# Optimization experiments

Measured on AMD Instinct MI355X. Metric: run time of the kernel, lower is better.

The kernel has to match this reference:

```python
import jax, jax.numpy as jnp
import numpy as np

LMAX=4; MMAX=2; L2=25; M2=19; C=64; CE=64; NRBF=600; CUT=5.0
HEADS=8; ACH=32; VCH=16; HMSG=64; HFF=128; G=288; NL=2
AVG_NEI=20.0; AVG_NODES=2000.0
N_NODES=2000; N_EDGES=40000; NSPEC=90
# |m| group of each truncated (edge-frame) coefficient, order l=0..4, m=-min(l,2)..min(l,2)
MG = np.array([0, 1,0,1, 2,1,0,1,2, 2,1,0,1,2, 2,1,0,1,2])
# l of each full SH coefficient (25 total)
LOC = np.array([0] + [1]*3 + [2]*5 + [3]*7 + [4]*9)

def silu(x):
    return x * jax.nn.sigmoid(x)

def rms_norm_sh(x, w):
    # x: [N, 25, C]; w: [5, C] per-degree affine weight (rms_norm_sh)
    ms = jnp.mean(x * x, axis=1, keepdims=True)
    return x * jax.lax.rsqrt(ms + 1e-6) * w[LOC][None]

def setup_inputs() -> dict:
    key = jax.random.key(0)
    ks = iter(jax.random.split(key, 64))
    def rn(shape, scale):
        return jax.random.normal(next(ks), shape, dtype=jnp.float32) * scale
    inp = {}
    inp['edge_vectors'] = rn((N_EDGES, 3), 1.5)
    inp['wigner'] = rn((N_EDGES, M2, L2), 0.2)
    inp['wigner_inv'] = rn((N_EDGES, L2, M2), 0.2)
    inp['species_embed'] = rn((NSPEC, C), 1.0)
    inp['edge_species_embed'] = rn((NSPEC, 2 * CE), 1.0)
    DIN = NRBF + 2 * CE  # 728
    inp['deg_W1'] = rn((DIN, 128), DIN ** -0.5)
    inp['deg_b1'] = jnp.zeros((128,), jnp.float32)
    inp['deg_W2'] = rn((128, M2 * C), 128 ** -0.5)
    inp['deg_b2'] = jnp.zeros((M2 * C,), jnp.float32)
    inp['norm1_w'] = jnp.ones((NL, 5, C), jnp.float32)
    inp['rad_W1'] = rn((NL, DIN, 128), DIN ** -0.5)
    inp['rad_b1'] = jnp.zeros((NL, 128), jnp.float32)
    inp['rad_W2'] = rn((NL, 128, 3 * 2 * C), 128 ** -0.5)
    inp['rad_b2'] = jnp.ones((NL, 3 * 2 * C), jnp.float32)
    inp['so2_W'] = rn((NL, 3, 2 * C, HMSG), (2 * C) ** -0.5)
    inp['alpha_W'] = rn((NL, HMSG, HEADS * ACH), HMSG ** -0.5)
    inp['alpha_vec'] = rn((NL, HEADS, ACH), ACH ** -0.5)
    inp['value_W'] = rn((NL, 3, HMSG, HEADS * VCH), HMSG ** -0.5)
    inp['proj_W'] = rn((NL, 3, HEADS * VCH, C), (HEADS * VCH) ** -0.5)
    inp['norm2_w'] = jnp.ones((NL, 5, C), jnp.float32)
    inp['ffn_W1'] = rn((NL, C, HFF), C ** -0.5)
    inp['ffn_b1'] = jnp.zeros((NL, HFF), jnp.float32)
    inp['ffn_W2'] = rn((NL, HFF, C), HFF ** -0.5)
    inp['to_grid'] = rn((G, L2), L2 ** -0.5)
    inp['from_grid'] = rn((L2, G), G ** -0.5)
    inp['final_norm_w'] = jnp.ones((5, C), jnp.float32)
    inp['en_W1'] = rn((C, HFF), C ** -0.5)
    inp['en_b1'] = jnp.zeros((HFF,), jnp.float32)
    inp['en_W2'] = rn((HFF, 1), HFF ** -0.5)
    inp['en_b2'] = jnp.zeros((1,), jnp.float32)
    inp['node_species'] = jax.random.randint(next(ks), (N_NODES,), 0, NSPEC, dtype=jnp.int32)
    inp['senders'] = jax.random.randint(next(ks), (N_EDGES,), 0, N_NODES, dtype=jnp.int32)
    inp['receivers'] = jax.random.randint(next(ks), (N_EDGES,), 0, N_NODES, dtype=jnp.int32)
    inp['n_node'] = jnp.array([N_NODES], jnp.int32)
    return inp

def reference(edge_vectors, wigner, wigner_inv, species_embed, edge_species_embed,
              deg_W1, deg_b1, deg_W2, deg_b2, norm1_w, rad_W1, rad_b1, rad_W2, rad_b2,
              so2_W, alpha_W, alpha_vec, value_W, proj_W, norm2_w, ffn_W1, ffn_b1, ffn_W2,
              to_grid, from_grid, final_norm_w, en_W1, en_b1, en_W2, en_b2,
              node_species, senders, receivers, n_node):
    N = node_species.shape[0]
    E = senders.shape[0]
    mg = jnp.asarray(MG)
    # Gaussian RBF distance expansion (rbf_width=2.0)
    d = jnp.sqrt(jnp.sum(edge_vectors * edge_vectors, axis=-1) + 1e-12)
    offs = jnp.linspace(0.0, CUT, NRBF)
    std = 2.0 * (CUT / (NRBF - 1))
    rbf = jnp.exp(-0.5 * ((d[:, None] - offs[None, :]) / std) ** 2)  # [E, 600]
    # shared atom-edge embedding concat
    ne = edge_species_embed[node_species]
    se, re = jnp.split(ne, 2, axis=-1)
    ee = jnp.concatenate([rbf, se[senders], re[receivers]], axis=1)  # [E, 728]
    # initial node features: species embedding on l=0 component
    x = jnp.zeros((N, L2, C), dtype=edge_vectors.dtype).at[:, 0, :].set(species_embed[node_species])
    # edge degree embedding: radial MLP -> edge-frame coeffs -> rotate back -> scatter
    h = silu(ee @ deg_W1 + deg_b1) @ deg_W2 + deg_b2
    deg = jnp.einsum('elm,emc->elc', wigner_inv, h.reshape(E, M2, C))  # [E,25,C]
    x = x + jax.ops.segment_sum(deg, receivers, num_segments=N) / AVG_NEI
    for i in range(NL):
        # --- SO2 equivariant graph attention ---
        res = x
        xn = rms_norm_sh(x, norm1_w[i])
        msg = jnp.concatenate([xn[senders], xn[receivers]], axis=-1)      # [E,25,2C]
        msg = jnp.einsum('eml,elc->emc', wigner, msg)                     # rotate to edge frame [E,19,2C]
        rad = (silu(ee @ rad_W1[i] + rad_b1[i]) @ rad_W2[i] + rad_b2[i]).reshape(E, MMAX + 1, 2 * C)
        msg = msg * rad[:, mg]                                            # per-|m| radial modulation
        h = jnp.einsum('emc,mco->emo', msg, so2_W[i][mg])                 # SO2 conv [E,19,HMSG]
        a = (silu(h[:, 0, :]) @ alpha_W[i]).reshape(E, HEADS, ACH)        # invariant (m=0) alpha path
        logits = jnp.sum(silu(a) * alpha_vec[i][None], axis=-1)           # [E,HEADS]
        mx = jax.ops.segment_max(logits, receivers, num_segments=N)[receivers]
        ex = jnp.exp(logits - mx)
        den = jax.ops.segment_sum(ex, receivers, num_segments=N)[receivers]
        attn = ex / (den + 1e-12)
        v = jnp.einsum('emo,mov->emv', h, value_W[i][mg]).reshape(E, M2, HEADS, VCH)
        v = (v * attn[:, None, :, None]).reshape(E, M2, HEADS * VCH)
        oe = jnp.einsum('emv,mvc->emc', v, proj_W[i][mg])                 # [E,19,C]
        oe = jnp.einsum('elm,emc->elc', wigner_inv, oe)                   # rotate back [E,25,C]
        x = res + jax.ops.segment_sum(oe, receivers, num_segments=N)
        # --- S2 grid feed-forward ---
        res = x
        xn = rms_norm_sh(x, norm2_w[i])
        g = jnp.einsum('gl,nlc->ngc', to_grid, xn)                        # [N,288,C]
        g = silu(g @ ffn_W1[i] + ffn_b1[i]) @ ffn_W2[i]
        x = res + jnp.einsum('lg,ngc->nlc', from_grid, g)
    # final norm + energy head
    xn = rms_norm_sh(x, final_norm_w)
    g = jnp.einsum('gl,nlc->ngc', to_grid, xn)
    g = silu(g @ en_W1 + en_b1) @ en_W2 + en_b2
    eo = jnp.einsum('lg,ngo->nlo', from_grid, g)
    return eo[:, 0, 0] / AVG_NODES
```

## Files before the change

kernel.cpp:

```cpp
#include <hip/hip_runtime.h>
#include <hip/hip_bf16.h>
#include <math.h>


#define NRBF 600
#define DIN 728
#define GPTS 288
#define CH 8

typedef __attribute__((ext_vector_type(8))) short bf16x8;
typedef __attribute__((ext_vector_type(4))) float f32x4;

__constant__ int d_mg[19] = {0,1,0,1,2,1,0,1,2,2,1,0,1,2,2,1,0,1,2};
__constant__ int d_loc[25] = {0,1,1,1,2,2,2,2,2,3,3,3,3,3,3,3,4,4,4,4,4,4,4,4,4};
__constant__ int d_mg0[5]={0,2,6,11,16};
__constant__ int d_mg1[8]={1,3,5,7,10,12,15,17};
__constant__ int d_mg2[6]={4,8,9,13,14,18};

__device__ inline float silu_f(float v){ return v/(1.0f+__expf(-v)); }
__device__ inline float bf2f(unsigned short u){ return __uint_as_float(((unsigned)u)<<16); }
__device__ inline unsigned short f2bf(float f){
  unsigned b=__float_as_uint(f);
  return (unsigned short)((b + 0x7FFF + ((b>>16)&1)) >> 16);
}

__device__ inline void atomicMaxF(float* addr, float val){
  int* ia=(int*)addr;
  int old=*ia;
  while (__int_as_float(old) < val){
    int assumed=old;
    old = atomicCAS(ia, assumed, __float_as_int(val));
    if (old == assumed) break;
  }
}

__global__ __launch_bounds__(256) void zero_cnt_kernel(int* cnt, int N){
  int i = blockIdx.x*256+threadIdx.x;
  if (i<N) cnt[i]=0;
}
__global__ __launch_bounds__(256) void csr_count_kernel(const int* __restrict__ rcv, int* cnt, int E){
  int i = blockIdx.x*256+threadIdx.x;
  if (i<E) atomicAdd(&cnt[rcv[i]],1);
}
__global__ __launch_bounds__(256) void csr_scan_kernel(const int* __restrict__ cnt,
    int* rowptr, int* fill, int N){
  __shared__ int s_part[256];
  int tid=threadIdx.x;
  int chunk=(N+255)/256;
  int lvals[12];
  int base=tid*chunk;
  int lsum=0;
  for (int i=0;i<chunk && i<12;i++){
    int v=(base+i<N)?cnt[base+i]:0;
    lvals[i]=lsum; lsum+=v;
  }
  s_part[tid]=lsum;
  __syncthreads();
  if (tid==0){
    int run=0;
    for (int t=0;t<256;t++){ int v=s_part[t]; s_part[t]=run; run+=v; }
  }
  __syncthreads();
  int off=s_part[tid];
  for (int i=0;i<chunk && i<12;i++){
    if (base+i<N){ rowptr[base+i]=off+lvals[i]; fill[base+i]=off+lvals[i]; }
  }
  if (tid==255) rowptr[N]=off+lsum;
}
__global__ __launch_bounds__(256) void csr_fill_kernel(const int* __restrict__ rcv,
    int* fill, int* eix, int E){
  int i = blockIdx.x*256+threadIdx.x;
  if (i<E){ int p=atomicAdd(&fill[rcv[i]],1); eix[p]=i; }
}

__global__ __launch_bounds__(256) void wsvb_kernel(const float* __restrict__ so2W,
    const float* __restrict__ valW, unsigned short* __restrict__ wsvb){
  int i=blockIdx.x/3, g=blockIdx.x%3;
  const float* A = so2W + (size_t)i*24576 + g*8192;
  const float* B = valW + (size_t)i*24576 + g*8192;
  unsigned short* C = wsvb + (size_t)blockIdx.x*16384;
  __shared__ float sB[8192];
  for (int j=threadIdx.x;j<2048;j+=256) ((float4*)sB)[j]=((const float4*)B)[j];
  __syncthreads();
  for (int idx=threadIdx.x; idx<16384; idx+=256){
    int k=idx>>7, j=idx&127;
    float acc=0;
    #pragma unroll 4
    for (int o=0;o<64;o++) acc += A[k*64+o]*sB[o*128+j];
    int pos = ((k>>5)*8 + (j>>4))*512 + (((k>>3)&3)*16 + (j&15))*8 + (k&7);
    C[pos]=f2bf(acc);
  }
}

__global__ __launch_bounds__(256) void projb_kernel(const float* __restrict__ pW,
    unsigned short* __restrict__ projb){
  const float* src = pW + (size_t)blockIdx.x*8192;
  unsigned short* dst = projb + (size_t)blockIdx.x*8192;
  for (int idx=threadIdx.x; idx<8192; idx+=256){
    int k=idx>>6, j=idx&63;
    int pos = ((k>>5)*4 + (j>>4))*512 + (((k>>3)&3)*16 + (j&15))*8 + (k&7);
    dst[pos]=f2bf(src[idx]);
  }
}

__global__ __launch_bounds__(256) void packB2g_kernel(const float* __restrict__ src,
    unsigned short* __restrict__ dh, unsigned short* __restrict__ dl, int K, int Nn){
  int ktiles=(K+31)>>5;
  int nnt=Nn>>4;
  int tot=ktiles*nnt*512;
  for (int idx=blockIdx.x*256+threadIdx.x; idx<tot; idx+=gridDim.x*256){
    int f=idx>>9, r=idx&511, lane=r>>3, j=r&7;
    int kt=f/nnt, nt=f-kt*nnt;
    int k=kt*32+(lane>>4)*8+j, c=nt*16+(lane&15);
    float v=(k<K)? src[k*Nn+c] : 0.0f;
    unsigned short h=f2bf(v);
    dh[idx]=h;
    dl[idx]=f2bf(v-bf2f(h));
  }
}

__global__ __launch_bounds__(256) void pack_tg2_kernel(const float* __restrict__ tg,
    unsigned short* __restrict__ tgp){
  int tid=threadIdx.x;
  for (int idx=tid; idx<9216; idx+=256){
    int t=idx>>9, r=idx&511, lane=r>>3, j=r&7;
    int kl=(lane>>4)*8+j, row=t*16+(lane&15);
    float v=(kl<25)? tg[row*25+kl] : 0.0f;
    unsigned short h=f2bf(v);
    tgp[idx]=h;
    tgp[9216+idx]=f2bf(v-bf2f(h));
  }
}

__global__ __launch_bounds__(256) void pack_fg2_kernel(const float* __restrict__ fg,
    unsigned short* __restrict__ fgp){
  int tid=threadIdx.x;
  for (int idx=tid; idx<18432; idx+=256){
    int f=idx>>9, r=idx&511, lane=r>>3, j=r&7;
    int t=f>>1, mt=f&1;
    int row=mt*16+(lane&15), k=(lane>>4)*8+j;
    float v=(row<25 && k<16)? fg[row*288+t*16+k] : 0.0f;
    unsigned short h=f2bf(v);
    fgp[idx]=h;
    fgp[18432+idx]=f2bf(v-bf2f(h));
  }
}

__global__ __launch_bounds__(256) void mlpf_kernel(const float* __restrict__ ev,
    const float* __restrict__ ese, const int* __restrict__ nsp,
    const unsigned short* __restrict__ dw1h, const unsigned short* __restrict__ dw1l,
    const float* __restrict__ db1,
    const unsigned short* __restrict__ dw2h, const unsigned short* __restrict__ dw2l,
    const float* __restrict__ db2,
    const unsigned short* __restrict__ r1h, const unsigned short* __restrict__ r1l,
    const float* __restrict__ rb1,
    const unsigned short* __restrict__ r2h, const unsigned short* __restrict__ r2l,
    const float* __restrict__ rb2,
    const int* __restrict__ snd, const int* __restrict__ rcv, const int* __restrict__ eix,
    int do_deg,
    unsigned short* __restrict__ degout, float* __restrict__ radout, int E){
  int tid=threadIdx.x, wv=tid>>6, lane=tid&63;
  int lanelo=lane&15, khi=lane>>4;
  int p0=blockIdx.x*16;
  __shared__ unsigned short s_eeh[4096], s_eel[4096];
  __shared__ unsigned short s_h1h[2048], s_h1l[2048];
  __shared__ float s_d[16]; __shared__ int s_ss[16], s_rs[16], s_e[16];
  if (tid<16){
    int p=p0+tid;
    int e=(p<E)? eix[p] : -1;
    s_e[tid]=e;
    if (e>=0){
      float vx=ev[3*e], vy=ev[3*e+1], vz=ev[3*e+2];
      s_d[tid]=sqrtf(vx*vx+vy*vy+vz*vz+1e-12f);
      s_ss[tid]=nsp[snd[e]]; s_rs[tid]=nsp[rcv[e]];
    } else { s_d[tid]=0.0f; s_ss[tid]=0; s_rs[tid]=0; }
  }
  __syncthreads();
  const float step=5.0f/599.0f, inv_std=1.0f/(2.0f*step);
  int nta=wv*2, ntb=nta+1;
  f32x4 z4={0,0,0,0};
  f32x4 aD0=z4,aD1=z4,aR0=z4,aR1=z4;
  for (int c=0;c<23;c+=CH){
    int ncur=23-c; if (ncur>CH) ncur=CH;
    for (int idx=tid; idx<ncur*512; idx+=256){
      int f=idx>>9, r=idx&511, ln=r>>3, j=r&7;
      int k=(c+f)*32+((ln>>4)<<3)+j, row=ln&15;
      float v=0.0f;
      if (k<NRBF){ float t=(s_d[row]-k*step)*inv_std; v=__expf(-0.5f*t*t); }
      else if (k<NRBF+64) v=ese[s_ss[row]*128+(k-NRBF)];
      else if (k<DIN)     v=ese[s_rs[row]*128+64+(k-NRBF-64)];
      unsigned short h=f2bf(v);
      s_eeh[idx]=h; s_eel[idx]=f2bf(v-bf2f(h));
    }
    __syncthreads();
    for (int f=0; f<ncur; f++){
      int kt=c+f;
      bf16x8 Ah=*(const bf16x8*)(s_eeh + f*512 + lane*8);
      bf16x8 Al=*(const bf16x8*)(s_eel + f*512 + lane*8);
      size_t ba=(size_t)(kt*8+nta)*512+lane*8;
      {
        bf16x8 Bh=*(const bf16x8*)(r1h+ba), Bl=*(const bf16x8*)(r1l+ba);
        bf16x8 Bh2=*(const bf16x8*)(r1h+ba+512), Bl2=*(const bf16x8*)(r1l+ba+512);
        aR0=__builtin_amdgcn_mfma_f32_16x16x32_bf16(Ah,Bh,aR0,0,0,0);
        aR0=__builtin_amdgcn_mfma_f32_16x16x32_bf16(Al,Bh,aR0,0,0,0);
        aR0=__builtin_amdgcn_mfma_f32_16x16x32_bf16(Ah,Bl,aR0,0,0,0);
        aR1=__builtin_amdgcn_mfma_f32_16x16x32_bf16(Ah,Bh2,aR1,0,0,0);
        aR1=__builtin_amdgcn_mfma_f32_16x16x32_bf16(Al,Bh2,aR1,0,0,0);
        aR1=__builtin_amdgcn_mfma_f32_16x16x32_bf16(Ah,Bl2,aR1,0,0,0);
      }
      if (do_deg){
        bf16x8 Bh=*(const bf16x8*)(dw1h+ba), Bl=*(const bf16x8*)(dw1l+ba);
        bf16x8 Bh2=*(const bf16x8*)(dw1h+ba+512), Bl2=*(const bf16x8*)(dw1l+ba+512);
        aD0=__builtin_amdgcn_mfma_f32_16x16x32_bf16(Ah,Bh,aD0,0,0,0);
        aD0=__builtin_amdgcn_mfma_f32_16x16x32_bf16(Al,Bh,aD0,0,0,0);
        aD0=__builtin_amdgcn_mfma_f32_16x16x32_bf16(Ah,Bl,aD0,0,0,0);
        aD1=__builtin_amdgcn_mfma_f32_16x16x32_bf16(Ah,Bh2,aD1,0,0,0);
        aD1=__builtin_amdgcn_mfma_f32_16x16x32_bf16(Al,Bh2,aD1,0,0,0);
        aD1=__builtin_amdgcn_mfma_f32_16x16x32_bf16(Ah,Bl2,aD1,0,0,0);
      }
    }
    __syncthreads();
  }
  int nmlp = do_deg ? 2 : 1;
  #pragma unroll 1
  for (int it=0; it<nmlp; it++){
    int is_deg = (it==1);
    f32x4 a0 = is_deg ? aD0 : aR0;
    f32x4 a1 = is_deg ? aD1 : aR1;
    const float* b1 = is_deg ? db1 : rb1;
    #pragma unroll
    for (int q=0;q<4;q++){
      int row=khi*4+q;
      {
        int col=nta*16+lanelo;
        float v=silu_f(a0[q]+b1[col]);
        int pos=row*128 + (((col>>3)^(row&7))<<3) + (col&7);
        unsigned short h=f2bf(v);
        s_h1h[pos]=h; s_h1l[pos]=f2bf(v-bf2f(h));
      }
      {
        int col=ntb*16+lanelo;
        float v=silu_f(a1[q]+b1[col]);
        int pos=row*128 + (((col>>3)^(row&7))<<3) + (col&7);
        unsigned short h=f2bf(v);
        s_h1h[pos]=h; s_h1l[pos]=f2bf(v-bf2f(h));
      }
    }
    __syncthreads();
    bf16x8 Ahh[4],Ahl[4];
    #pragma unroll
    for (int kt=0;kt<4;kt++){
      int o=lanelo*128 + (((kt*4+khi)^(lanelo&7))<<3);
      Ahh[kt]=*(const bf16x8*)(s_h1h+o);
      Ahl[kt]=*(const bf16x8*)(s_h1l+o);
    }
    __syncthreads();
    if (is_deg){
      for (int nt=wv; nt<76; nt+=4){
        f32x4 acc=z4;
        #pragma unroll
        for (int kt=0;kt<4;kt++){
          size_t bo=(size_t)(kt*76+nt)*512+lane*8;
          bf16x8 Bh=*(const bf16x8*)(dw2h+bo), Bl=*(const bf16x8*)(dw2l+bo);
          acc=__builtin_amdgcn_mfma_f32_16x16x32_bf16(Ahh[kt],Bh,acc,0,0,0);
          acc=__builtin_amdgcn_mfma_f32_16x16x32_bf16(Ahl[kt],Bh,acc,0,0,0);
          acc=__builtin_amdgcn_mfma_f32_16x16x32_bf16(Ahh[kt],Bl,acc,0,0,0);
        }
        int col=nt*16+lanelo;
        float bb=db2[col];
        #pragma unroll
        for (int q=0;q<4;q++){
          int p=p0+khi*4+q;
          if (p<E) degout[(size_t)p*1216+col]=f2bf(acc[q]+bb);
        }
      }
    } else {
      for (int nt=wv; nt<24; nt+=4){
        f32x4 acc=z4;
        #pragma unroll
        for (int kt=0;kt<4;kt++){
          size_t bo=(size_t)(kt*24+nt)*512+lane*8;
          bf16x8 Bh=*(const bf16x8*)(r2h+bo), Bl=*(const bf16x8*)(r2l+bo);
          acc=__builtin_amdgcn_mfma_f32_16x16x32_bf16(Ahh[kt],Bh,acc,0,0,0);
          acc=__builtin_amdgcn_mfma_f32_16x16x32_bf16(Ahl[kt],Bh,acc,0,0,0);
          acc=__builtin_amdgcn_mfma_f32_16x16x32_bf16(Ahh[kt],Bl,acc,0,0,0);
        }
        int col=nt*16+lanelo;
        float bb=rb2[col];
        #pragma unroll
        for (int q=0;q<4;q++){
          int e=s_e[khi*4+q];
          if (e>=0) radout[(size_t)e*384+col]=acc[q]+bb;
        }
      }
    }
  }
}

__global__ __launch_bounds__(256) void deg_sum_kernel(const unsigned short* __restrict__ h2,
    const float* __restrict__ winv, const int* __restrict__ rowptr, const int* __restrict__ eix,
    const int* __restrict__ nsp, const float* __restrict__ spe,
    float* __restrict__ x, int N){
  int n=blockIdx.x, tid=threadIdx.x;
  __shared__ float s_winv[475];
  __shared__ unsigned short s_oe[1216];
  int row0=rowptr[n];
  int cnt=rowptr[n+1]-row0;
  float4 acc0={0,0,0,0}, acc1={0,0,0,0};
  int it1=tid+256;
  for (int j=0;j<cnt;j++){
    int p=row0+j;
    int e=eix[p];
    for (int k2=tid;k2<475;k2+=256) s_winv[k2]=winv[(size_t)e*475+k2];
    for (int k2=tid;k2<152;k2+=256) ((int4*)s_oe)[k2]=((const int4*)(h2+(size_t)p*1216))[k2];
    __syncthreads();
    const unsigned* o2=(const unsigned*)s_oe;
    {
      int l=tid>>4, c4=tid&15;
      const float* wr=s_winv+l*19;
      #pragma unroll
      for (int m=0;m<19;m++){
        float w=wr[m];
        unsigned ua=o2[m*32+c4*2], ub=o2[m*32+c4*2+1];
        acc0.x+=w*bf2f((unsigned short)(ua&0xffffu));
        acc0.y+=w*bf2f((unsigned short)(ua>>16));
        acc0.z+=w*bf2f((unsigned short)(ub&0xffffu));
        acc0.w+=w*bf2f((unsigned short)(ub>>16));
      }
    }
    if (it1<400){
      int l=it1>>4, c4=it1&15;
      const float* wr=s_winv+l*19;
      #pragma unroll
      for (int m=0;m<19;m++){
        float w=wr[m];
        unsigned ua=o2[m*32+c4*2], ub=o2[m*32+c4*2+1];
        acc1.x+=w*bf2f((unsigned short)(ua&0xffffu));
        acc1.y+=w*bf2f((unsigned short)(ua>>16));
        acc1.z+=w*bf2f((unsigned short)(ub&0xffffu));
        acc1.w+=w*bf2f((unsigned short)(ub>>16));
      }
    }
    __syncthreads();
  }
  int sp=nsp[n];
  const float4* sp4=(const float4*)(spe+(size_t)sp*64);
  float4* xp=(float4*)(x+(size_t)n*1600);
  {
    int l=tid>>4, c4=tid&15;
    float4 base=(l==0)? sp4[c4] : make_float4(0,0,0,0);
    float4 o;
    o.x=base.x+0.05f*acc0.x; o.y=base.y+0.05f*acc0.y;
    o.z=base.z+0.05f*acc0.z; o.w=base.w+0.05f*acc0.w;
    xp[tid]=o;
  }
  if (it1<400){
    float4 o;
    o.x=0.05f*acc1.x; o.y=0.05f*acc1.y; o.z=0.05f*acc1.z; o.w=0.05f*acc1.w;
    xp[it1]=o;
  }
}

__global__ __launch_bounds__(256) void rmsnorm_kernel(const float* __restrict__ x,
    const float* __restrict__ w, float* __restrict__ xn, int N){
  int n = blockIdx.x, tid = threadIdx.x;
  __shared__ float s_x[1600];
  __shared__ float s_part[256];
  __shared__ float s_ms[64];
  const float* xr = x + (size_t)n*1600;
  for (int j=tid;j<1600;j+=256) s_x[j]=xr[j];
  __syncthreads();
  {
    int c = tid&63, seg = tid>>6;
    float acc=0;
    for (int l=seg;l<25;l+=4){ float v=s_x[l*64+c]; acc+=v*v; }
    s_part[tid]=acc;
  }
  __syncthreads();
  if (tid<64){
    float m=(s_part[tid]+s_part[tid+64]+s_part[tid+128]+s_part[tid+192])*(1.0f/25.0f);
    s_ms[tid]=rsqrtf(m+1e-6f);
  }
  __syncthreads();
  float* xo = xn + (size_t)n*1600;
  for (int j=tid;j<1600;j+=256){
    int l=j>>6, c=j&63;
    xo[j]=s_x[j]*s_ms[c]*w[d_loc[l]*64+c];
  }
}

__global__ __launch_bounds__(256) void init_mxden_kernel(float* mx, float* den, int N){
  int idx = blockIdx.x*256+threadIdx.x;
  if (idx < N*8){ mx[idx]=-3.0e38f; den[idx]=0.0f; }
}

__global__ __launch_bounds__(256) void logits_kernel(const float* __restrict__ xn,
    const float* __restrict__ wig, const float* __restrict__ radb,
    const float* __restrict__ so2W, const float* __restrict__ alphaW, const float* __restrict__ alphaV,
    const int* __restrict__ snd, const int* __restrict__ rcv,
    float* __restrict__ logits, float* __restrict__ mx, int E){
  int e = blockIdx.x, tid = threadIdx.x;
  __shared__ float s_cat[3200];
  __shared__ float s_wig0[25];
  __shared__ float s_msg0[128];
  __shared__ float s_sh0[64];
  __shared__ float s_a[256];
  int s = snd[e], r = rcv[e];
  const float4* xs4 = (const float4*)(xn + (size_t)s*1600);
  const float4* xr4 = (const float4*)(xn + (size_t)r*1600);
  float4* cat4 = (float4*)s_cat;
  for (int j=tid;j<400;j+=256){
    int l=j>>4, c4=j&15;
    cat4[l*32+c4]    = xs4[j];
    cat4[l*32+16+c4] = xr4[j];
  }
  if (tid<25) s_wig0[tid]=wig[(size_t)e*475+tid];
  __syncthreads();
  if (tid<128){
    float acc=0;
    #pragma unroll
    for (int l=0;l<25;l++) acc += s_wig0[l]*s_cat[l*128+tid];
    s_msg0[tid]=acc*radb[(size_t)e*384+tid];
  }
  __syncthreads();
  if (tid<64){
    float acc=0;
    #pragma unroll
    for (int k=0;k<128;k++) acc += s_msg0[k]*so2W[k*64+tid];
    s_sh0[tid]=silu_f(acc);
  }
  __syncthreads();
  {
    float acc=0;
    #pragma unroll
    for (int o=0;o<64;o++) acc += s_sh0[o]*alphaW[o*256+tid];
    s_a[tid]=silu_f(acc)*alphaV[tid];
  }
  __syncthreads();
  if (tid<8){
    float lg=0;
    #pragma unroll
    for (int q=0;q<32;q++) lg += s_a[tid*32+q];
    logits[(size_t)e*8+tid]=lg;
    atomicMaxF(&mx[r*8+tid], lg);
  }
}

__global__ __launch_bounds__(256) void den_kernel(const float* __restrict__ logits,
    const float* __restrict__ mx, const int* __restrict__ rcv,
    float* __restrict__ den, int E){
  int idx = blockIdx.x*256+threadIdx.x;
  if (idx >= E*8) return;
  int e = idx>>3, hd = idx&7, r = rcv[e];
  atomicAdd(&den[r*8+hd], __expf(logits[idx]-mx[r*8+hd]));
}

__global__ __launch_bounds__(256) void msg_kernel(const float* __restrict__ xn,
    const float* __restrict__ wig, const float* __restrict__ radb,
    const int* __restrict__ snd, const int* __restrict__ rcv, const int* __restrict__ eix,
    unsigned short* __restrict__ msgb, int E){
  __shared__ float s_wig[1900];
  int tid=threadIdx.x, wv=tid>>6, lane=tid&63;
  int p=blockIdx.x*4+wv;
  bool act=(p<E);
  int pc=act? p : (E-1);
  int e=eix[pc];
  int node=(lane<32)? snd[e] : rcv[e];
  int c2=(lane&31)*2;
  int col0=c2+((lane>>5)<<6);
  const float* xb=xn+(size_t)node*1600+c2;
  float ca[25], cb[25];
  #pragma unroll
  for (int l=0;l<25;l++){
    float2 v=*(const float2*)(xb+l*64);
    ca[l]=v.x; cb[l]=v.y;
  }
  float* swig=s_wig+wv*475;
  for (int j=lane;j<475;j+=64) swig[j]=wig[(size_t)e*475+j];
  float ra0,ra1,rb0,rb1,rc0,rc1;
  {
    const float* rb_=radb+(size_t)e*384;
    float2 v0=*(const float2*)(rb_+col0);
    float2 v1=*(const float2*)(rb_+128+col0);
    float2 v2=*(const float2*)(rb_+256+col0);
    ra0=v0.x; ra1=v0.y; rb0=v1.x; rb1=v1.y; rc0=v2.x; rc1=v2.y;
  }
  __syncthreads();
  unsigned short* dst=msgb+(size_t)pc*2432+col0;
  constexpr int mgc[19]={0,1,0,1,2,1,0,1,2,2,1,0,1,2,2,1,0,1,2};
  if (act){
    #pragma unroll
    for (int m=0;m<19;m++){
      float a0=0.0f,a1=0.0f;
      const float* wr=swig+m*25;
      #pragma unroll
      for (int l=0;l<25;l++){ float w=wr[l]; a0+=w*ca[l]; a1+=w*cb[l]; }
      float r0,r1;
      if (mgc[m]==0){ r0=ra0; r1=ra1; }
      else if (mgc[m]==1){ r0=rb0; r1=rb1; }
      else { r0=rc0; r1=rc1; }
      a0*=r0; a1*=r1;
      unsigned packv=((unsigned)f2bf(a1)<<16)|(unsigned)f2bf(a0);
      *(unsigned*)(dst+m*128)=packv;
    }
  }
}

__global__ __launch_bounds__(256) void attn_gemm_kernel(unsigned short* __restrict__ msgb,
    const unsigned short* __restrict__ wsvp, const unsigned short* __restrict__ projp,
    const float* __restrict__ logits, const float* __restrict__ mx, const float* __restrict__ den,
    const int* __restrict__ eix, const int* __restrict__ rcv, int E){
  int tid=threadIdx.x, wv=tid>>6, lane=tid&63;
  int lanelo=lane&15, khi=lane>>4;
  int p0=blockIdx.x*16;
  __shared__ unsigned short s_vv[2176];
  __shared__ float s_attn[16][8];
  __shared__ short s_r2e[304], s_r2m[304];
  for (int j=tid;j<304;j+=256){
    int e,m;
    if (j<80){ e=j/5; m=d_mg0[j%5]; }
    else if (j<208){ int q=j-80; e=q>>3; m=d_mg1[q&7]; }
    else { int q=j-208; e=q/6; m=d_mg2[q%6]; }
    s_r2e[j]=(short)e; s_r2m[j]=(short)m;
  }
  if (tid<128){
    int i=tid>>3, h=tid&7, p=p0+i;
    float a=0.0f;
    if (p<E){
      int e=eix[p]; int r=rcv[e];
      a=__expf(logits[(size_t)e*8+h]-mx[r*8+h])/(den[r*8+h]+1e-12f);
    }
    s_attn[i][h]=a;
  }
  __syncthreads();
  const int4* wp4=(const int4*)wsvp;
  const int4* pp4=(const int4*)projp;
  for (int t=0;t<19;t++){
    int g=(t<5)?0:((t<13)?1:2);
    int R=t*16+lanelo;
    int ei=s_r2e[R], mi=s_r2m[R];
    int pp=p0+ei;
    size_t abase=((size_t)((pp<E)?pp:0))*2432 + (size_t)mi*128;
    bf16x8 A[4];
    #pragma unroll
    for (int kt=0;kt<4;kt++)
      A[kt]=*(const bf16x8*)(msgb + abase + kt*32 + khi*8);
    #pragma unroll
    for (int h2=0;h2<2;h2++){
      int nt=wv*2+h2;
      f32x4 acc={0,0,0,0};
      #pragma unroll
      for (int kt=0;kt<4;kt++){
        int4 tt=wp4[g*2048+(kt*8+nt)*64+lane];
        acc=__builtin_amdgcn_mfma_f32_16x16x32_bf16(A[kt],*(bf16x8*)&tt,acc,0,0,0);
      }
      int col=nt*16+lanelo;
      #pragma unroll
      for (int q=0;q<4;q++){
        int r16=khi*4+q;
        int ei2=s_r2e[t*16+r16];
        s_vv[r16*136+col]=f2bf(acc[q]*s_attn[ei2][nt]);
      }
    }
    __syncthreads();
    {
      bf16x8 A2[4];
      #pragma unroll
      for (int kt=0;kt<4;kt++)
        A2[kt]=*(const bf16x8*)(s_vv + lanelo*136 + kt*32 + khi*8);
      f32x4 acc={0,0,0,0};
      #pragma unroll
      for (int kt=0;kt<4;kt++){
        int4 tt=pp4[g*1024+(kt*4+wv)*64+lane];
        acc=__builtin_amdgcn_mfma_f32_16x16x32_bf16(A2[kt],*(bf16x8*)&tt,acc,0,0,0);
      }
      int col=wv*16+lanelo;
      #pragma unroll
      for (int q=0;q<4;q++){
        int R2=t*16+khi*4+q;
        int pi=p0+s_r2e[R2];
        if (pi<E) msgb[(size_t)pi*2432 + (size_t)s_r2m[R2]*128 + col]=f2bf(acc[q]);
      }
    }
    __syncthreads();
  }
}

__global__ __launch_bounds__(256) void attn_sum_kernel(const unsigned short* __restrict__ msgb,
    const float* __restrict__ winv, const int* __restrict__ rowptr, const int* __restrict__ eix,
    float* __restrict__ x, int N){
  int n=blockIdx.x, tid=threadIdx.x;
  __shared__ float s_winv[475];
  __shared__ unsigned short s_oe[1216];
  int row0=rowptr[n];
  int cnt=rowptr[n+1]-row0;
  float4 acc0={0,0,0,0}, acc1={0,0,0,0};
  int it1=tid+256;
  for (int j=0;j<cnt;j++){
    int p=row0+j;
    int e=eix[p];
    for (int k2=tid;k2<475;k2+=256) s_winv[k2]=winv[(size_t)e*475+k2];
    for (int k2=tid;k2<152;k2+=256){
      int m=k2>>3, jj=k2&7;
      ((int4*)s_oe)[k2]=*(const int4*)(msgb + (size_t)p*2432 + m*128 + jj*8);
    }
    __syncthreads();
    const unsigned* o2=(const unsigned*)s_oe;
    {
      int l=tid>>4, c4=tid&15;
      const float* wr=s_winv+l*19;
      #pragma unroll
      for (int m=0;m<19;m++){
        float w=wr[m];
        unsigned ua=o2[m*32+c4*2], ub=o2[m*32+c4*2+1];
        acc0.x+=w*bf2f((unsigned short)(ua&0xffffu));
        acc0.y+=w*bf2f((unsigned short)(ua>>16));
        acc0.z+=w*bf2f((unsigned short)(ub&0xffffu));
        acc0.w+=w*bf2f((unsigned short)(ub>>16));
      }
    }
    if (it1<400){
      int l=it1>>4, c4=it1&15;
      const float* wr=s_winv+l*19;
      #pragma unroll
      for (int m=0;m<19;m++){
        float w=wr[m];
        unsigned ua=o2[m*32+c4*2], ub=o2[m*32+c4*2+1];
        acc1.x+=w*bf2f((unsigned short)(ua&0xffffu));
        acc1.y+=w*bf2f((unsigned short)(ua>>16));
        acc1.z+=w*bf2f((unsigned short)(ub&0xffffu));
        acc1.w+=w*bf2f((unsigned short)(ub>>16));
      }
    }
    __syncthreads();
  }
  float4* xp=(float4*)(x+(size_t)n*1600);
  {
    float4 c=xp[tid];
    c.x+=acc0.x; c.y+=acc0.y; c.z+=acc0.z; c.w+=acc0.w;
    xp[tid]=c;
  }
  if (it1<400){
    float4 c=xp[it1];
    c.x+=acc1.x; c.y+=acc1.y; c.z+=acc1.z; c.w+=acc1.w;
    xp[it1]=c;
  }
}

__global__ __launch_bounds__(256) void grid_ffn_mfma_kernel(const float* __restrict__ xn,
    const unsigned short* __restrict__ tgp, const unsigned short* __restrict__ fgp,
    const unsigned short* __restrict__ w1p, const unsigned short* __restrict__ w2p,
    const float* __restrict__ b1, float* __restrict__ x, int N){
  int n=blockIdx.x, tid=threadIdx.x, wv=tid>>6, lane=tid&63;
  int lanelo=lane&15, khi=lane>>4;
  __shared__ __align__(16) char s_mem[74240];
  unsigned short* s_w1=(unsigned short*)s_mem;
  unsigned short* s_xn=(unsigned short*)(s_mem+32768);
  float* s_b1=(float*)(s_mem+40960);
  unsigned short* scr=(unsigned short*)(s_mem+41472)+(size_t)wv*4096;
  for (int j=tid;j<2048;j+=256) ((int4*)s_w1)[j]=((const int4*)w1p)[j];
  if (tid<128) s_b1[tid]=b1[tid];
  { int4 z={0,0,0,0}; for (int j=tid;j<512;j+=256) ((int4*)s_xn)[j]=z; }
  __syncthreads();
  {
    const float* xr=xn+(size_t)n*1600;
    for (int j=tid;j<1600;j+=256){
      int k=j>>6, c=j&63;
      float v=xr[j];
      unsigned short h=f2bf(v);
      s_xn[c*32+k]=h;
      s_xn[2048+c*32+k]=f2bf(v-bf2f(h));
    }
  }
  __syncthreads();
  bf16x8 XBh[4],XBl[4];
  #pragma unroll
  for (int ct=0;ct<4;ct++){
    int o=(ct*16+lanelo)*32 + khi*8;
    XBh[ct]=*(const bf16x8*)(s_xn+o);
    XBl[ct]=*(const bf16x8*)(s_xn+2048+o);
  }
  f32x4 oacc[2][4];
  #pragma unroll
  for (int mt=0;mt<2;mt++)
    #pragma unroll
    for (int nt=0;nt<4;nt++){ f32x4 z={0,0,0,0}; oacc[mt][nt]=z; }
  for (int t=wv;t<18;t+=4){
    bf16x8 Atgh=*(const bf16x8*)(tgp + t*512 + lane*8);
    bf16x8 Atgl=*(const bf16x8*)(tgp + 9216 + t*512 + lane*8);
    #pragma unroll
    for (int ct=0;ct<4;ct++){
      f32x4 g={0,0,0,0};
      g=__builtin_amdgcn_mfma_f32_16x16x32_bf16(Atgh,XBh[ct],g,0,0,0);
      g=__builtin_amdgcn_mfma_f32_16x16x32_bf16(Atgl,XBh[ct],g,0,0,0);
      g=__builtin_amdgcn_mfma_f32_16x16x32_bf16(Atgh,XBl[ct],g,0,0,0);
      #pragma unroll
      for (int q=0;q<4;q++){
        int row=khi*4+q, col=ct*16+lanelo;
        int pos=row*64 + (((col>>3)^(row&7))<<3) + (col&7);
        float v=g[q]; unsigned short h=f2bf(v);
        scr[pos]=h; scr[1024+pos]=f2bf(v-bf2f(h));
      }
    }
    bf16x8 Agh[2],Agl[2];
    #pragma unroll
    for (int kt=0;kt<2;kt++){
      int o=lanelo*64 + (((kt*4+khi)^(lanelo&7))<<3);
      Agh[kt]=*(const bf16x8*)(scr+o);
      Agl[kt]=*(const bf16x8*)(scr+1024+o);
    }
    #pragma unroll
    for (int nt=0;nt<8;nt++){
      f32x4 h={0,0,0,0};
      #pragma unroll
      for (int kt=0;kt<2;kt++){
        bf16x8 Bh=*(const bf16x8*)(s_w1 + (kt*8+nt)*512 + lane*8);
        bf16x8 Bl=*(const bf16x8*)(s_w1 + 8192 + (kt*8+nt)*512 + lane*8);
        h=__builtin_amdgcn_mfma_f32_16x16x32_bf16(Agh[kt],Bh,h,0,0,0);
        h=__builtin_amdgcn_mfma_f32_16x16x32_bf16(Agl[kt],Bh,h,0,0,0);
        h=__builtin_amdgcn_mfma_f32_16x16x32_bf16(Agh[kt],Bl,h,0,0,0);
      }
      #pragma unroll
      for (int q=0;q<4;q++){
        int row=khi*4+q, col=nt*16+lanelo;
        float v=silu_f(h[q]+s_b1[col]);
        int pos=row*128 + (((col>>3)^(row&7))<<3) + (col&7);
        unsigned short hh=f2bf(v);
        scr[pos]=hh; scr[2048+pos]=f2bf(v-bf2f(hh));
      }
    }
    bf16x8 Ahh[4],Ahl[4];
    #pragma unroll
    for (int kt=0;kt<4;kt++){
      int o=lanelo*128 + (((kt*4+khi)^(lanelo&7))<<3);
      Ahh[kt]=*(const bf16x8*)(scr+o);
      Ahl[kt]=*(const bf16x8*)(scr+2048+o);
    }
    #pragma unroll
    for (int nt=0;nt<4;nt++){
      f32x4 o4={0,0,0,0};
      #pragma unroll
      for (int kt=0;kt<4;kt++){
        bf16x8 Bh=*(const bf16x8*)(w2p + (kt*4+nt)*512 + lane*8);
        bf16x8 Bl=*(const bf16x8*)(w2p + 8192 + (kt*4+nt)*512 + lane*8);
        o4=__builtin_amdgcn_mfma_f32_16x16x32_bf16(Ahh[kt],Bh,o4,0,0,0);
        o4=__builtin_amdgcn_mfma_f32_16x16x32_bf16(Ahl[kt],Bh,o4,0,0,0);
        o4=__builtin_amdgcn_mfma_f32_16x16x32_bf16(Ahh[kt],Bl,o4,0,0,0);
      }
      #pragma unroll
      for (int q=0;q<4;q++){
        int ch=nt*16+lanelo, rowk=khi*4+q;
        int pos=ch*32 + (((rowk>>3)^(ch&3))<<3) + (rowk&7);
        float v=o4[q]; unsigned short hh=f2bf(v);
        scr[pos]=hh; scr[2048+pos]=f2bf(v-bf2f(hh));
      }
    }
    bf16x8 Boh[4],Bol[4];
    #pragma unroll
    for (int nt=0;nt<4;nt++){
      int ch=nt*16+lanelo;
      int o=ch*32 + ((khi^(ch&3))<<3);
      Boh[nt]=*(const bf16x8*)(scr+o);
      Bol[nt]=*(const bf16x8*)(scr+2048+o);
    }
    #pragma unroll
    for (int mt=0;mt<2;mt++){
      bf16x8 Afh=*(const bf16x8*)(fgp + (t*2+mt)*512 + lane*8);
      bf16x8 Afl=*(const bf16x8*)(fgp + 18432 + (t*2+mt)*512 + lane*8);
      #pragma unroll
      for (int nt=0;nt<4;nt++){
        oacc[mt][nt]=__builtin_amdgcn_mfma_f32_16x16x32_bf16(Afh,Boh[nt],oacc[mt][nt],0,0,0);
        oacc[mt][nt]=__builtin_amdgcn_mfma_f32_16x16x32_bf16(Afl,Boh[nt],oacc[mt][nt],0,0,0);
        oacc[mt][nt]=__builtin_amdgcn_mfma_f32_16x16x32_bf16(Afh,Bol[nt],oacc[mt][nt],0,0,0);
      }
    }
  }
  __syncthreads();
  float* pout=(float*)s_mem;
  #pragma unroll
  for (int mt=0;mt<2;mt++)
    #pragma unroll
    for (int nt=0;nt<4;nt++)
      #pragma unroll
      for (int q=0;q<4;q++){
        int row=mt*16+khi*4+q, col=nt*16+lanelo;
        pout[wv*2048 + row*64 + col]=oacc[mt][nt][q];
      }
  __syncthreads();
  for (int j=tid;j<1600;j+=256)
    x[(size_t)n*1600+j] += pout[j]+pout[2048+j]+pout[4096+j]+pout[6144+j];
}

__global__ __launch_bounds__(256) void energy_mfma_kernel(const float* __restrict__ xn,
    const unsigned short* __restrict__ tgp, const float* __restrict__ fg,
    const unsigned short* __restrict__ enw1p, const float* __restrict__ b1,
    const float* __restrict__ w2, const float* __restrict__ b2,
    float* __restrict__ out, int N){
  int n=blockIdx.x, tid=threadIdx.x, wv=tid>>6, lane=tid&63;
  int lanelo=lane&15, khi=lane>>4;
  __shared__ __align__(16) char s_mem[59584];
  unsigned short* s_w1=(unsigned short*)s_mem;
  unsigned short* s_xn=(unsigned short*)(s_mem+32768);
  float* s_b1=(float*)(s_mem+40960);
  float* s_w2=(float*)(s_mem+41472);
  float* s_fg0=(float*)(s_mem+41984);
  float* s_red=(float*)(s_mem+43136);
  unsigned short* scr=(unsigned short*)(s_mem+43200)+(size_t)wv*2048;
  for (int j=tid;j<2048;j+=256) ((int4*)s_w1)[j]=((const int4*)enw1p)[j];
  if (tid<128){ s_b1[tid]=b1[tid]; s_w2[tid]=w2[tid]; }
  for (int j=tid;j<288;j+=256) s_fg0[j]=fg[j];
  { int4 z={0,0,0,0}; for (int j=tid;j<512;j+=256) ((int4*)s_xn)[j]=z; }
  __syncthreads();
  {
    const float* xr=xn+(size_t)n*1600;
    for (int j=tid;j<1600;j+=256){
      int k=j>>6, c=j&63;
      float v=xr[j];
      unsigned short h=f2bf(v);
      s_xn[c*32+k]=h;
      s_xn[2048+c*32+k]=f2bf(v-bf2f(h));
    }
  }
  __syncthreads();
  bf16x8 XBh[4],XBl[4];
  #pragma unroll
  for (int ct=0;ct<4;ct++){
    int o=(ct*16+lanelo)*32 + khi*8;
    XBh[ct]=*(const bf16x8*)(s_xn+o);
    XBl[ct]=*(const bf16x8*)(s_xn+2048+o);
  }
  float b2v=b2[0];
  float e=0.0f;
  for (int t=wv;t<18;t+=4){
    bf16x8 Atgh=*(const bf16x8*)(tgp + t*512 + lane*8);
    bf16x8 Atgl=*(const bf16x8*)(tgp + 9216 + t*512 + lane*8);
    #pragma unroll
    for (int ct=0;ct<4;ct++){
      f32x4 g={0,0,0,0};
      g=__builtin_amdgcn_mfma_f32_16x16x32_bf16(Atgh,XBh[ct],g,0,0,0);
      g=__builtin_amdgcn_mfma_f32_16x16x32_bf16(Atgl,XBh[ct],g,0,0,0);
      g=__builtin_amdgcn_mfma_f32_16x16x32_bf16(Atgh,XBl[ct],g,0,0,0);
      #pragma unroll
      for (int q=0;q<4;q++){
        int row=khi*4+q, col=ct*16+lanelo;
        int pos=row*64 + (((col>>3)^(row&7))<<3) + (col&7);
        float v=g[q]; unsigned short h=f2bf(v);
        scr[pos]=h; scr[1024+pos]=f2bf(v-bf2f(h));
      }
    }
    bf16x8 Agh[2],Agl[2];
    #pragma unroll
    for (int kt=0;kt<2;kt++){
      int o=lanelo*64 + (((kt*4+khi)^(lanelo&7))<<3);
      Agh[kt]=*(const bf16x8*)(scr+o);
      Agl[kt]=*(const bf16x8*)(scr+1024+o);
    }
    #pragma unroll
    for (int nt=0;nt<8;nt++){
      f32x4 h={0,0,0,0};
      #pragma unroll
      for (int kt=0;kt<2;kt++){
        bf16x8 Bh=*(const bf16x8*)(s_w1 + (kt*8+nt)*512 + lane*8);
        bf16x8 Bl=*(const bf16x8*)(s_w1 + 8192 + (kt*8+nt)*512 + lane*8);
        h=__builtin_amdgcn_mfma_f32_16x16x32_bf16(Agh[kt],Bh,h,0,0,0);
        h=__builtin_amdgcn_mfma_f32_16x16x32_bf16(Agl[kt],Bh,h,0,0,0);
        h=__builtin_amdgcn_mfma_f32_16x16x32_bf16(Agh[kt],Bl,h,0,0,0);
      }
      #pragma unroll
      for (int q=0;q<4;q++){
        int row=khi*4+q, col=nt*16+lanelo;
        float v=silu_f(h[q]+s_b1[col]);
        e += v*s_w2[col]*s_fg0[t*16+row];
      }
    }
    if (lanelo==0){
      #pragma unroll
      for (int q=0;q<4;q++) e += s_fg0[t*16+khi*4+q]*b2v;
    }
  }
  #pragma unroll
  for (int d=1;d<64;d<<=1) e += __shfl_xor(e,d);
  if (lane==0) s_red[wv]=e;
  __syncthreads();
  if (tid==0) out[n]=(s_red[0]+s_red[1]+s_red[2]+s_red[3])*(1.0f/2000.0f);
}

extern "C" void kernel_launch(void* const* d_in, const int* in_sizes, int n_in,
                              void* d_out, int out_size, void* d_ws, size_t ws_size,
                              hipStream_t stream){
  (void)n_in; (void)out_size; (void)ws_size;
  const float* ev   = (const float*)d_in[0];
  const float* wig  = (const float*)d_in[1];
  const float* winv = (const float*)d_in[2];
  const float* spe  = (const float*)d_in[3];
  const float* ese  = (const float*)d_in[4];
  const float* degW1= (const float*)d_in[5];
  const float* degb1= (const float*)d_in[6];
  const float* degW2= (const float*)d_in[7];
  const float* degb2= (const float*)d_in[8];
  const float* n1w  = (const float*)d_in[9];
  const float* radW1= (const float*)d_in[10];
  const float* radb1= (const float*)d_in[11];
  const float* radW2= (const float*)d_in[12];
  const float* radb2= (const float*)d_in[13];
  const float* so2W = (const float*)d_in[14];
  const float* aW   = (const float*)d_in[15];
  const float* aV   = (const float*)d_in[16];
  const float* vW   = (const float*)d_in[17];
  const float* pW   = (const float*)d_in[18];
  const float* n2w  = (const float*)d_in[19];
  const float* fW1  = (const float*)d_in[20];
  const float* fb1  = (const float*)d_in[21];
  const float* fW2  = (const float*)d_in[22];
  const float* tg   = (const float*)d_in[23];
  const float* fg   = (const float*)d_in[24];
  const float* fnw  = (const float*)d_in[25];
  const float* enW1 = (const float*)d_in[26];
  const float* enb1 = (const float*)d_in[27];
  const float* enW2 = (const float*)d_in[28];
  const float* enb2 = (const float*)d_in[29];
  const int* nsp = (const int*)d_in[30];
  const int* snd = (const int*)d_in[31];
  const int* rcv = (const int*)d_in[32];
  int N = in_sizes[30];
  int E = in_sizes[31];
  float* out = (float*)d_out;

  float* ws = (float*)d_ws;
  size_t off = 0;
  float* radbuf = ws + off; off += (size_t)E*384;
  float* logits = ws + off; off += (size_t)E*8;
  float* mx     = ws + off; off += (size_t)N*8;
  float* den    = ws + off; off += (size_t)N*8;
  float* x      = ws + off; off += (size_t)N*1600;
  float* xn     = ws + off; off += (size_t)N*1600;
  unsigned short* wsvb  = (unsigned short*)(ws + off); off += (size_t)6*16384/2;
  unsigned short* projb = (unsigned short*)(ws + off); off += (size_t)6*8192/2;
  int* cnt      = (int*)(ws + off); off += (size_t)N;
  int* rowptr   = (int*)(ws + off); off += (size_t)(N+1);
  int* fill     = (int*)(ws + off); off += (size_t)N;
  int* eixbuf   = (int*)(ws + off); off += (size_t)E;
  off = (off + 3) & ~((size_t)3);
  unsigned short* msgb  = (unsigned short*)(ws + off); off += (size_t)E*1216;
  unsigned short* tgp   = (unsigned short*)(ws + off); off += 9216;
  unsigned short* fgp   = (unsigned short*)(ws + off); off += 18432;
  unsigned short* wwp   = (unsigned short*)(ws + off); off += 32768;
  unsigned short* enw1p = (unsigned short*)(ws + off); off += 8192;
  unsigned short* degw1p = (unsigned short*)(ws + off); off += 94208;
  unsigned short* degw2p = (unsigned short*)(ws + off); off += 155648;
  unsigned short* radw1p = (unsigned short*)(ws + off); off += 94208*2;
  unsigned short* radw2p = (unsigned short*)(ws + off); off += 49152*2;

  zero_cnt_kernel<<<(N+255)/256, 256, 0, stream>>>(cnt, N);
  csr_count_kernel<<<(E+255)/256, 256, 0, stream>>>(rcv, cnt, E);
  csr_scan_kernel<<<1, 256, 0, stream>>>(cnt, rowptr, fill, N);
  csr_fill_kernel<<<(E+255)/256, 256, 0, stream>>>(rcv, fill, eixbuf, E);
  wsvb_kernel<<<6, 256, 0, stream>>>(so2W, vW, wsvb);
  projb_kernel<<<6, 256, 0, stream>>>(pW, projb);
  pack_tg2_kernel<<<1, 256, 0, stream>>>(tg, tgp);
  pack_fg2_kernel<<<1, 256, 0, stream>>>(fg, fgp);
  for (int i=0;i<2;i++){
    unsigned short* wl = wwp + (size_t)i*32768;
    packB2g_kernel<<<8, 256, 0, stream>>>(fW1 + (size_t)i*8192, wl, wl+8192, 64, 128);
    packB2g_kernel<<<8, 256, 0, stream>>>(fW2 + (size_t)i*8192, wl+16384, wl+24576, 128, 64);
  }
  packB2g_kernel<<<8, 256, 0, stream>>>(enW1, enw1p, enw1p+8192, 64, 128);
  packB2g_kernel<<<32, 256, 0, stream>>>(degW1, degw1p, degw1p+94208, DIN, 128);
  packB2g_kernel<<<32, 256, 0, stream>>>(degW2, degw2p, degw2p+155648, 128, 1216);
  for (int i=0;i<2;i++){
    unsigned short* r1 = radw1p + (size_t)i*188416;
    unsigned short* r2 = radw2p + (size_t)i*98304;
    packB2g_kernel<<<32, 256, 0, stream>>>(radW1 + (size_t)i*DIN*128, r1, r1+94208, DIN, 128);
    packB2g_kernel<<<16, 256, 0, stream>>>(radW2 + (size_t)i*128*384, r2, r2+49152, 128, 384);
  }

  mlpf_kernel<<<(E+15)/16, 256, 0, stream>>>(ev, ese, nsp,
      degw1p, degw1p+94208, degb1, degw2p, degw2p+155648, degb2,
      radw1p, radw1p+94208, radb1,
      radw2p, radw2p+49152, radb2,
      snd, rcv, eixbuf, 1, msgb, radbuf, E);
  deg_sum_kernel<<<N, 256, 0, stream>>>(msgb, winv, rowptr, eixbuf, nsp, spe, x, N);

  for (int i=0;i<2;i++){
    if (i==1){
      unsigned short* r1 = radw1p + (size_t)188416;
      unsigned short* r2 = radw2p + (size_t)98304;
      mlpf_kernel<<<(E+15)/16, 256, 0, stream>>>(ev, ese, nsp,
          degw1p, degw1p+94208, degb1, degw2p, degw2p+155648, degb2,
          r1, r1+94208, radb1+128,
          r2, r2+49152, radb2+384,
          snd, rcv, eixbuf, 0, msgb, radbuf, E);
    }
    rmsnorm_kernel<<<N, 256, 0, stream>>>(x, n1w + (size_t)i*320, xn, N);
    init_mxden_kernel<<<(N*8+255)/256, 256, 0, stream>>>(mx, den, N);
    logits_kernel<<<E, 256, 0, stream>>>(xn, wig, radbuf, so2W + (size_t)i*24576,
                                         aW + (size_t)i*64*256, aV + (size_t)i*256,
                                         snd, rcv, logits, mx, E);
    den_kernel<<<(E*8+255)/256, 256, 0, stream>>>(logits, mx, rcv, den, E);
    msg_kernel<<<(E+3)/4, 256, 0, stream>>>(xn, wig, radbuf, snd, rcv, eixbuf, msgb, E);
    attn_gemm_kernel<<<(E+15)/16, 256, 0, stream>>>(msgb,
                                                    wsvb + (size_t)i*3*16384, projb + (size_t)i*3*8192,
                                                    logits, mx, den, eixbuf, rcv, E);
    attn_sum_kernel<<<N, 256, 0, stream>>>(msgb, winv, rowptr, eixbuf, x, N);
    rmsnorm_kernel<<<N, 256, 0, stream>>>(x, n2w + (size_t)i*320, xn, N);
    grid_ffn_mfma_kernel<<<N, 256, 0, stream>>>(xn, tgp, fgp,
                                                wwp + (size_t)i*32768, wwp + (size_t)i*32768 + 16384,
                                                fb1 + (size_t)i*128, x, N);
  }
  rmsnorm_kernel<<<N, 256, 0, stream>>>(x, fnw, xn, N);
  energy_mfma_kernel<<<N, 256, 0, stream>>>(xn, tgp, fg, enw1p, enb1, enW2, enb2, out, N);
}
```

Baseline: 2.938 ms.

## Split node edge-sum across waves with per-wave LDS buffers and final reduction

The two per-node gather kernels (degree embedding and attention output) are merged into one kernel with a mode flag. Each of the four waves now handles every fourth incoming edge, staging that edge's rotation matrix and message in its own shared-memory slot. This removes the two block-wide barriers per edge, and each wave keeps 7 float4 accumulators covering all 400 outputs. The partial sums are reduced across waves through shared memory at the end, at the cost of more registers and shared memory per block.

```diff
diff --git a/kernel.cpp b/kernel.cpp
--- a/kernel.cpp
+++ b/kernel.cpp
@@ -297,67 +297,87 @@
   }
 }
 
-__global__ __launch_bounds__(256) void deg_sum_kernel(const unsigned short* __restrict__ h2,
+__global__ __launch_bounds__(256) void node_sum_kernel(const unsigned short* __restrict__ msgb,
     const float* __restrict__ winv, const int* __restrict__ rowptr, const int* __restrict__ eix,
     const int* __restrict__ nsp, const float* __restrict__ spe,
-    float* __restrict__ x, int N){
-  int n=blockIdx.x, tid=threadIdx.x;
-  __shared__ float s_winv[475];
-  __shared__ unsigned short s_oe[1216];
+    float* __restrict__ x, int mode, int N){
+  int n=blockIdx.x, tid=threadIdx.x, wv=tid>>6, lane=tid&63;
+  __shared__ float s_winv[4][480];
+  __shared__ unsigned short s_oe[4][1216];
+  __shared__ float4 s_red[4][400];
   int row0=rowptr[n];
   int cnt=rowptr[n+1]-row0;
-  float4 acc0={0,0,0,0}, acc1={0,0,0,0};
-  int it1=tid+256;
-  for (int j=0;j<cnt;j++){
+  float4 acc[7];
+  #pragma unroll
+  for (int t=0;t<7;t++) acc[t]=make_float4(0,0,0,0);
+  for (int j=wv; j<cnt; j+=4){
     int p=row0+j;
     int e=eix[p];
-    for (int k2=tid;k2<475;k2+=256) s_winv[k2]=winv[(size_t)e*475+k2];
-    for (int k2=tid;k2<152;k2+=256) ((int4*)s_oe)[k2]=((const int4*)(h2+(size_t)p*1216))[k2];
-    __syncthreads();
-    const unsigned* o2=(const unsigned*)s_oe;
-    {
-      int l=tid>>4, c4=tid&15;
-      const float* wr=s_winv+l*19;
-      #pragma unroll
-      for (int m=0;m<19;m++){
-        float w=wr[m];
-        unsigned ua=o2[m*32+c4*2], ub=o2[m*32+c4*2+1];
-        acc0.x+=w*bf2f((unsigned short)(ua&0xffffu));
-        acc0.y+=w*bf2f((unsigned short)(ua>>16));
-        acc0.z+=w*bf2f((unsigned short)(ub&0xffffu));
-        acc0.w+=w*bf2f((unsigned short)(ub>>16));
-      }
-    }
-    if (it1<400){
-      int l=it1>>4, c4=it1&15;
-      const float* wr=s_winv+l*19;
-      #pragma unroll
-      for (int m=0;m<19;m++){
-        float w=wr[m];
-        unsigned ua=o2[m*32+c4*2], ub=o2[m*32+c4*2+1];
-        acc1.x+=w*bf2f((unsigned short)(ua&0xffffu));
-        acc1.y+=w*bf2f((unsigned short)(ua>>16));
-        acc1.z+=w*bf2f((unsigned short)(ub&0xffffu));
-        acc1.w+=w*bf2f((unsigned short)(ub>>16));
-      }
-    }
-    __syncthreads();
-  }
-  int sp=nsp[n];
-  const float4* sp4=(const float4*)(spe+(size_t)sp*64);
+    asm volatile("s_waitcnt lgkmcnt(0)" ::: "memory");
+    for (int k=lane;k<475;k+=64) s_winv[wv][k]=winv[(size_t)e*475+k];
+    if (mode==1){
+      for (int k=lane;k<152;k+=64)
+        ((int4*)s_oe[wv])[k]=*(const int4*)(msgb+(size_t)p*1216+k*8);
+    } else {
+      for (int k=lane;k<152;k+=64){
+        int m=k>>3, jj=k&7;
+        ((int4*)s_oe[wv])[k]=*(const int4*)(msgb+(size_t)p*2432+m*128+jj*8);
+      }
+    }
+    asm volatile("s_waitcnt lgkmcnt(0)" ::: "memory");
+    const unsigned* o2=(const unsigned*)s_oe[wv];
+    #pragma unroll
+    for (int t=0;t<7;t++){
+      int sI=lane+t*64;
+      if (sI<400){
+        int l=sI>>4, c4=sI&15;
+        const float* wr=s_winv[wv]+l*19;
+        float4 a=acc[t];
+        #pragma unroll
+        for (int m=0;m<19;m++){
+          float w=wr[m];
+          unsigned ua=o2[m*32+c4*2], ub=o2[m*32+c4*2+1];
+          a.x+=w*bf2f((unsigned short)(ua&0xffffu));
+          a.y+=w*bf2f((unsigned short)(ua>>16));
+          a.z+=w*bf2f((unsigned short)(ub&0xffffu));
+          a.w+=w*bf2f((unsigned short)(ub>>16));
+        }
+        acc[t]=a;
+      }
+    }
+  }
+  asm volatile("s_waitcnt lgkmcnt(0)" ::: "memory");
+  #pragma unroll
+  for (int t=0;t<7;t++){
+    int sI=lane+t*64;
+    if (sI<400) s_red[wv][sI]=acc[t];
+  }
+  __syncthreads();
   float4* xp=(float4*)(x+(size_t)n*1600);
-  {
-    int l=tid>>4, c4=tid&15;
-    float4 base=(l==0)? sp4[c4] : make_float4(0,0,0,0);
-    float4 o;
-    o.x=base.x+0.05f*acc0.x; o.y=base.y+0.05f*acc0.y;
-    o.z=base.z+0.05f*acc0.z; o.w=base.w+0.05f*acc0.w;
-    xp[tid]=o;
-  }
-  if (it1<400){
-    float4 o;
-    o.x=0.05f*acc1.x; o.y=0.05f*acc1.y; o.z=0.05f*acc1.z; o.w=0.05f*acc1.w;
-    xp[it1]=o;
+  if (mode==0){
+    for (int j=tid;j<400;j+=256){
+      float4 a=s_red[0][j], b=s_red[1][j], c=s_red[2][j], d=s_red[3][j];
+      float4 cur=xp[j];
+      cur.x+=a.x+b.x+c.x+d.x;
+      cur.y+=a.y+b.y+c.y+d.y;
+      cur.z+=a.z+b.z+c.z+d.z;
+      cur.w+=a.w+b.w+c.w+d.w;
+      xp[j]=cur;
+    }
+  } else {
+    int sp=nsp[n];
+    const float4* sp4=(const float4*)(spe+(size_t)sp*64);
+    for (int j=tid;j<400;j+=256){
+      int l=j>>4, c4=j&15;
+      float4 a=s_red[0][j], b=s_red[1][j], c=s_red[2][j], d=s_red[3][j];
+      float4 base=(l==0)? sp4[c4] : make_float4(0,0,0,0);
+      float4 o;
+      o.x=base.x+0.05f*(a.x+b.x+c.x+d.x);
+      o.y=base.y+0.05f*(a.y+b.y+c.y+d.y);
+      o.z=base.z+0.05f*(a.z+b.z+c.z+d.z);
+      o.w=base.w+0.05f*(a.w+b.w+c.w+d.w);
+      xp[j]=o;
+    }
   }
 }
 
@@ -583,67 +603,6 @@
       }
     }
     __syncthreads();
-  }
-}
-
-__global__ __launch_bounds__(256) void attn_sum_kernel(const unsigned short* __restrict__ msgb,
-    const float* __restrict__ winv, const int* __restrict__ rowptr, const int* __restrict__ eix,
-    float* __restrict__ x, int N){
-  int n=blockIdx.x, tid=threadIdx.x;
-  __shared__ float s_winv[475];
-  __shared__ unsigned short s_oe[1216];
-  int row0=rowptr[n];
-  int cnt=rowptr[n+1]-row0;
-  float4 acc0={0,0,0,0}, acc1={0,0,0,0};
-  int it1=tid+256;
-  for (int j=0;j<cnt;j++){
-    int p=row0+j;
-    int e=eix[p];
-    for (int k2=tid;k2<475;k2+=256) s_winv[k2]=winv[(size_t)e*475+k2];
-    for (int k2=tid;k2<152;k2+=256){
-      int m=k2>>3, jj=k2&7;
-      ((int4*)s_oe)[k2]=*(const int4*)(msgb + (size_t)p*2432 + m*128 + jj*8);
-    }
-    __syncthreads();
-    const unsigned* o2=(const unsigned*)s_oe;
-    {
-      int l=tid>>4, c4=tid&15;
-      const float* wr=s_winv+l*19;
-      #pragma unroll
-      for (int m=0;m<19;m++){
-        float w=wr[m];
-        unsigned ua=o2[m*32+c4*2], ub=o2[m*32+c4*2+1];
-        acc0.x+=w*bf2f((unsigned short)(ua&0xffffu));
-        acc0.y+=w*bf2f((unsigned short)(ua>>16));
-        acc0.z+=w*bf2f((unsigned short)(ub&0xffffu));
-        acc0.w+=w*bf2f((unsigned short)(ub>>16));
-      }
-    }
-    if (it1<400){
-      int l=it1>>4, c4=it1&15;
-      const float* wr=s_winv+l*19;
-      #pragma unroll
-      for (int m=0;m<19;m++){
-        float w=wr[m];
-        unsigned ua=o2[m*32+c4*2], ub=o2[m*32+c4*2+1];
-        acc1.x+=w*bf2f((unsigned short)(ua&0xffffu));
-        acc1.y+=w*bf2f((unsigned short)(ua>>16));
-        acc1.z+=w*bf2f((unsigned short)(ub&0xffffu));
-        acc1.w+=w*bf2f((unsigned short)(ub>>16));
-      }
-    }
-    __syncthreads();
-  }
-  float4* xp=(float4*)(x+(size_t)n*1600);
-  {
-    float4 c=xp[tid];
-    c.x+=acc0.x; c.y+=acc0.y; c.z+=acc0.z; c.w+=acc0.w;
-    xp[tid]=c;
-  }
-  if (it1<400){
-    float4 c=xp[it1];
-    c.x+=acc1.x; c.y+=acc1.y; c.z+=acc1.z; c.w+=acc1.w;
-    xp[it1]=c;
   }
 }
 
@@ -979,7 +938,7 @@
       radw1p, radw1p+94208, radb1,
       radw2p, radw2p+49152, radb2,
       snd, rcv, eixbuf, 1, msgb, radbuf, E);
-  deg_sum_kernel<<<N, 256, 0, stream>>>(msgb, winv, rowptr, eixbuf, nsp, spe, x, N);
+  node_sum_kernel<<<N, 256, 0, stream>>>(msgb, winv, rowptr, eixbuf, nsp, spe, x, 1, N);
 
   for (int i=0;i<2;i++){
     if (i==1){
@@ -1001,7 +960,7 @@
     attn_gemm_kernel<<<(E+15)/16, 256, 0, stream>>>(msgb,
                                                     wsvb + (size_t)i*3*16384, projb + (size_t)i*3*8192,
                                                     logits, mx, den, eixbuf, rcv, E);
-    attn_sum_kernel<<<N, 256, 0, stream>>>(msgb, winv, rowptr, eixbuf, x, N);
+    node_sum_kernel<<<N, 256, 0, stream>>>(msgb, winv, rowptr, eixbuf, nsp, spe, x, 0, N);
     rmsnorm_kernel<<<N, 256, 0, stream>>>(x, n2w + (size_t)i*320, xn, N);
     grid_ffn_mfma_kernel<<<N, 256, 0, stream>>>(xn, tgp, fgp,
                                                 wwp + (size_t)i*32768, wwp + (size_t)i*32768 + 16384,
```

New measurement: 2.790 ms. 5.0% less time.
